# Kernel optimization log

Measured on AMD Instinct MI355X. Metric: run time of the kernel, lower is better.

Reference implementation:

```python
import jax, jax.numpy as jnp
import numpy as np

MIN_DISTANCE = 1.0  # default forward arg of the torch module


def setup_inputs() -> dict:
    key = jax.random.key(0)
    k1, k2 = jax.random.split(key)
    B, N = 4, 4096
    coords = jax.random.normal(k1, (B, N, 3), dtype=jnp.float32) * 5.0
    steric_radii = jax.random.uniform(k2, (B, N), dtype=jnp.float32)
    return {"coords": coords, "steric_radii": steric_radii}


def reference(coords, steric_radii):
    # coords: [B,N,3], steric_radii: [B,N]
    diff = coords[:, :, None, :] - coords[:, None, :, :]          # [B,N,N,3]
    d2 = jnp.sum(diff * diff, axis=-1)                             # [B,N,N]
    # safe sqrt: exact 0 on the diagonal (matches torch.cdist), no NaN grads
    pairwise = jnp.where(d2 > 0, jnp.sqrt(jnp.where(d2 > 0, d2, 1.0)), 0.0)
    sr = steric_radii[:, :, None] + steric_radii[:, None, :]       # [B,N,N]
    target = jnp.maximum(MIN_DISTANCE, sr)
    penalty = jax.nn.relu(target - pairwise)[..., None]            # [B,N,N,1]
    direction = jnp.clip(diff, -1.0, 1.0)                          # [B,N,N,3]
    adjustment = jnp.mean(penalty * direction, axis=2)             # [B,N,3]
    return coords + 0.1 * adjustment
```

## Files before the change

### kernel.cpp

```cpp
#include <hip/hip_runtime.h>

#define BB 4
#define NN 4096
#define TI 256
#define JB 32
#define JLEN (NN / JB)

#if __has_builtin(__builtin_amdgcn_sqrtf)
  #define FAST_SQRT __builtin_amdgcn_sqrtf
#else
  #define FAST_SQRT sqrtf
#endif

__device__ __forceinline__ float clip1(float x) {
    return fminf(fmaxf(x, -1.0f), 1.0f);
}

__global__ __launch_bounds__(TI) void ncp_partial(
    const float* __restrict__ coords,
    const float* __restrict__ radii,
    float* __restrict__ part)
{
    __shared__ float4 jt[JLEN];
    const int b = blockIdx.z;
    const int i = blockIdx.x * TI + threadIdx.x;
    const int s = blockIdx.y;
    const int jbase = s * JLEN;

    if (threadIdx.x < JLEN) {
        const int jj = jbase + threadIdx.x;
        jt[threadIdx.x] = make_float4(coords[(b * NN + jj) * 3 + 0],
                                      coords[(b * NN + jj) * 3 + 1],
                                      coords[(b * NN + jj) * 3 + 2],
                                      radii[b * NN + jj]);
    }

    const float xi = coords[(b * NN + i) * 3 + 0];
    const float yi = coords[(b * NN + i) * 3 + 1];
    const float zi = coords[(b * NN + i) * 3 + 2];
    const float ri = radii[b * NN + i];

    float ax = 0.0f, ay = 0.0f, az = 0.0f;

    __syncthreads();

    #pragma unroll 4
    for (int k = 0; k < JLEN; ++k) {
        const float4 c = jt[k];
        const float dx = xi - c.x;
        const float dy = yi - c.y;
        const float dz = zi - c.z;
        const float d2 = fmaf(dx, dx, fmaf(dy, dy, dz * dz));
        if (__any(d2 < 4.0f)) {
            const float dist = FAST_SQRT(d2);
            const float tgt = fmaxf(1.0f, ri + c.w);
            const float p = fmaxf(tgt - dist, 0.0f);
            ax = fmaf(p, clip1(dx), ax);
            ay = fmaf(p, clip1(dy), ay);
            az = fmaf(p, clip1(dz), az);
        }
    }

    float* dst = part + (size_t)s * (BB * NN * 3);
    const int o = (b * NN + i) * 3;
    dst[o + 0] = ax;
    dst[o + 1] = ay;
    dst[o + 2] = az;
}

__global__ __launch_bounds__(256) void ncp_reduce(
    const float* __restrict__ coords,
    const float* __restrict__ part,
    float* __restrict__ out)
{
    const int o = blockIdx.x * 256 + threadIdx.x;
    if (o >= BB * NN * 3) return;
    float acc = 0.0f;
    #pragma unroll
    for (int s = 0; s < JB; ++s)
        acc += part[(size_t)s * (BB * NN * 3) + o];
    out[o] = fmaf(0.1f / (float)NN, acc, coords[o]);
}

__global__ __launch_bounds__(TI) void ncp_direct(
    const float* __restrict__ coords,
    const float* __restrict__ radii,
    float* __restrict__ out)
{
    __shared__ float4 jt[TI];
    const int b = blockIdx.z;
    const int i = blockIdx.x * TI + threadIdx.x;

    const float xi = coords[(b * NN + i) * 3 + 0];
    const float yi = coords[(b * NN + i) * 3 + 1];
    const float zi = coords[(b * NN + i) * 3 + 2];
    const float ri = radii[b * NN + i];

    float ax = 0.0f, ay = 0.0f, az = 0.0f;

    for (int jc = 0; jc < NN; jc += TI) {
        const int jj = jc + threadIdx.x;
        __syncthreads();
        jt[threadIdx.x] = make_float4(coords[(b * NN + jj) * 3 + 0],
                                      coords[(b * NN + jj) * 3 + 1],
                                      coords[(b * NN + jj) * 3 + 2],
                                      radii[b * NN + jj]);
        __syncthreads();
        #pragma unroll 4
        for (int k = 0; k < TI; ++k) {
            const float4 c = jt[k];
            const float dx = xi - c.x;
            const float dy = yi - c.y;
            const float dz = zi - c.z;
            const float d2 = fmaf(dx, dx, fmaf(dy, dy, dz * dz));
            if (__any(d2 < 4.0f)) {
                const float dist = FAST_SQRT(d2);
                const float tgt = fmaxf(1.0f, ri + c.w);
                const float p = fmaxf(tgt - dist, 0.0f);
                ax = fmaf(p, clip1(dx), ax);
                ay = fmaf(p, clip1(dy), ay);
                az = fmaf(p, clip1(dz), az);
            }
        }
    }

    const int o = (b * NN + i) * 3;
    const float sc = 0.1f / (float)NN;
    out[o + 0] = fmaf(sc, ax, coords[o + 0]);
    out[o + 1] = fmaf(sc, ay, coords[o + 1]);
    out[o + 2] = fmaf(sc, az, coords[o + 2]);
}

extern "C" void kernel_launch(void* const* d_in, const int* in_sizes, int n_in,
                              void* d_out, int out_size, void* d_ws, size_t ws_size,
                              hipStream_t stream) {
    const float* coords = (const float*)d_in[0];
    const float* radii  = (const float*)d_in[1];
    float* out = (float*)d_out;
    const int n = BB * NN * 3;
    const size_t need = (size_t)JB * n * sizeof(float);

    if (ws_size >= need) {
        ncp_partial<<<dim3(NN / TI, JB, BB), TI, 0, stream>>>(
            coords, radii, (float*)d_ws);
        ncp_reduce<<<(n + 255) / 256, 256, 0, stream>>>(
            coords, (float*)d_ws, out);
    } else {
        ncp_direct<<<dim3(NN / TI, 1, BB), TI, 0, stream>>>(coords, radii, out);
    }
}
```

Before: 81.14 us.

## Pre-pack coords and radii into float4 buffer and read j-tiles directly from global

Adds a pack kernel that interleaves coords and radii into a float4 workspace array. The partial kernel then reads j-points straight from global memory through uniform float4 loads instead of staging them in LDS behind a __syncthreads. This removes the strided three-float gathers and the block barrier, at the cost of an extra kernel launch and more workspace use. Inner-loop loads now hit the cache instead of LDS.

```diff
diff --git a/kernel.cpp b/kernel.cpp
--- a/kernel.cpp
+++ b/kernel.cpp
@@ -16,37 +16,37 @@
     return fminf(fmaxf(x, -1.0f), 1.0f);
 }
 
-__global__ __launch_bounds__(TI) void ncp_partial(
+#define PACK_ELEMS (BB * NN)
+#define PART_OFF   (PACK_ELEMS * 4)
+
+__global__ __launch_bounds__(256) void ncp_pack(
     const float* __restrict__ coords,
     const float* __restrict__ radii,
+    float4* __restrict__ packed)
+{
+    const int t = blockIdx.x * 256 + threadIdx.x;
+    if (t >= PACK_ELEMS) return;
+    packed[t] = make_float4(coords[t * 3 + 0], coords[t * 3 + 1],
+                            coords[t * 3 + 2], radii[t]);
+}
+
+__global__ __launch_bounds__(TI) void ncp_partial(
+    const float4* __restrict__ packed,
     float* __restrict__ part)
 {
-    __shared__ float4 jt[JLEN];
     const int b = blockIdx.z;
     const int i = blockIdx.x * TI + threadIdx.x;
     const int s = blockIdx.y;
-    const int jbase = s * JLEN;
+    const float4* jsrc = packed + b * NN + s * JLEN;
 
-    if (threadIdx.x < JLEN) {
-        const int jj = jbase + threadIdx.x;
-        jt[threadIdx.x] = make_float4(coords[(b * NN + jj) * 3 + 0],
-                                      coords[(b * NN + jj) * 3 + 1],
-                                      coords[(b * NN + jj) * 3 + 2],
-                                      radii[b * NN + jj]);
-    }
-
-    const float xi = coords[(b * NN + i) * 3 + 0];
-    const float yi = coords[(b * NN + i) * 3 + 1];
-    const float zi = coords[(b * NN + i) * 3 + 2];
-    const float ri = radii[b * NN + i];
+    const float4 me = packed[b * NN + i];
+    const float xi = me.x, yi = me.y, zi = me.z, ri = me.w;
 
     float ax = 0.0f, ay = 0.0f, az = 0.0f;
 
-    __syncthreads();
-
     #pragma unroll 4
     for (int k = 0; k < JLEN; ++k) {
-        const float4 c = jt[k];
+        const float4 c = jsrc[k];
         const float dx = xi - c.x;
         const float dy = yi - c.y;
         const float dz = zi - c.z;
@@ -138,13 +138,14 @@
     const float* radii  = (const float*)d_in[1];
     float* out = (float*)d_out;
     const int n = BB * NN * 3;
-    const size_t need = (size_t)JB * n * sizeof(float);
+    const size_t need = (size_t)(PART_OFF + (size_t)JB * n) * sizeof(float);
 
     if (ws_size >= need) {
-        ncp_partial<<<dim3(NN / TI, JB, BB), TI, 0, stream>>>(
-            coords, radii, (float*)d_ws);
-        ncp_reduce<<<(n + 255) / 256, 256, 0, stream>>>(
-            coords, (float*)d_ws, out);
+        float4* packed = (float4*)d_ws;
+        float* part = (float*)d_ws + PART_OFF;
+        ncp_pack<<<(PACK_ELEMS + 255) / 256, 256, 0, stream>>>(coords, radii, packed);
+        ncp_partial<<<dim3(NN / TI, JB, BB), TI, 0, stream>>>(packed, part);
+        ncp_reduce<<<(n + 255) / 256, 256, 0, stream>>>(coords, part, out);
     } else {
         ncp_direct<<<dim3(NN / TI, 1, BB), TI, 0, stream>>>(coords, radii, out);
     }
```

Measured after the change: 81.12 us. About the same (-0.0%).

## Fuse partial and reduce kernels into one block-level j-split with shared-memory reduction

Applied to the files above, without the earlier changes.

Replaces the two-kernel scheme (per-slice partial sums to workspace, then a reduce kernel) with a single kernel. Each 1024-thread block stages all 4096 points of a batch in LDS, handles 32 i-points, and splits j across 32 half-wave streams. The partial sums are then combined in shared memory. This removes the second launch and the global workspace traffic, and makes each wavefront's __any branch cover only 32 i-points against contiguous j. The cost is that every block reloads the full 64KB point set, only 96 threads do the final reduction, and a 64KB LDS footprint plus large blocks may limit occupancy.

```diff
diff --git a/kernel.cpp b/kernel.cpp
--- a/kernel.cpp
+++ b/kernel.cpp
@@ -2,9 +2,10 @@
 
 #define BB 4
 #define NN 4096
-#define TI 256
-#define JB 32
-#define JLEN (NN / JB)
+#define TPB 1024
+#define STREAMS 32
+#define JPS (NN / STREAMS)
+#define GRP 4
 
 #if __has_builtin(__builtin_amdgcn_sqrtf)
   #define FAST_SQRT __builtin_amdgcn_sqrtf
@@ -16,107 +17,53 @@
     return fminf(fmaxf(x, -1.0f), 1.0f);
 }
 
-__global__ __launch_bounds__(TI) void ncp_partial(
-    const float* __restrict__ coords,
-    const float* __restrict__ radii,
-    float* __restrict__ part)
-{
-    __shared__ float4 jt[JLEN];
-    const int b = blockIdx.z;
-    const int i = blockIdx.x * TI + threadIdx.x;
-    const int s = blockIdx.y;
-    const int jbase = s * JLEN;
-
-    if (threadIdx.x < JLEN) {
-        const int jj = jbase + threadIdx.x;
-        jt[threadIdx.x] = make_float4(coords[(b * NN + jj) * 3 + 0],
-                                      coords[(b * NN + jj) * 3 + 1],
-                                      coords[(b * NN + jj) * 3 + 2],
-                                      radii[b * NN + jj]);
-    }
-
-    const float xi = coords[(b * NN + i) * 3 + 0];
-    const float yi = coords[(b * NN + i) * 3 + 1];
-    const float zi = coords[(b * NN + i) * 3 + 2];
-    const float ri = radii[b * NN + i];
-
-    float ax = 0.0f, ay = 0.0f, az = 0.0f;
-
-    __syncthreads();
-
-    #pragma unroll 4
-    for (int k = 0; k < JLEN; ++k) {
-        const float4 c = jt[k];
-        const float dx = xi - c.x;
-        const float dy = yi - c.y;
-        const float dz = zi - c.z;
-        const float d2 = fmaf(dx, dx, fmaf(dy, dy, dz * dz));
-        if (__any(d2 < 4.0f)) {
-            const float dist = FAST_SQRT(d2);
-            const float tgt = fmaxf(1.0f, ri + c.w);
-            const float p = fmaxf(tgt - dist, 0.0f);
-            ax = fmaf(p, clip1(dx), ax);
-            ay = fmaf(p, clip1(dy), ay);
-            az = fmaf(p, clip1(dz), az);
-        }
-    }
-
-    float* dst = part + (size_t)s * (BB * NN * 3);
-    const int o = (b * NN + i) * 3;
-    dst[o + 0] = ax;
-    dst[o + 1] = ay;
-    dst[o + 2] = az;
-}
-
-__global__ __launch_bounds__(256) void ncp_reduce(
-    const float* __restrict__ coords,
-    const float* __restrict__ part,
-    float* __restrict__ out)
-{
-    const int o = blockIdx.x * 256 + threadIdx.x;
-    if (o >= BB * NN * 3) return;
-    float acc = 0.0f;
-    #pragma unroll
-    for (int s = 0; s < JB; ++s)
-        acc += part[(size_t)s * (BB * NN * 3) + o];
-    out[o] = fmaf(0.1f / (float)NN, acc, coords[o]);
-}
-
-__global__ __launch_bounds__(TI) void ncp_direct(
+__global__ __launch_bounds__(TPB, 8) void ncp_one(
     const float* __restrict__ coords,
     const float* __restrict__ radii,
     float* __restrict__ out)
 {
-    __shared__ float4 jt[TI];
+    __shared__ __align__(16) char smem[65536];
+    float4* pts = (float4*)smem;
+    float*  red = (float*)smem;
+
     const int b = blockIdx.z;
-    const int i = blockIdx.x * TI + threadIdx.x;
+    const int ibase = blockIdx.x * 32;
 
-    const float xi = coords[(b * NN + i) * 3 + 0];
-    const float yi = coords[(b * NN + i) * 3 + 1];
-    const float zi = coords[(b * NN + i) * 3 + 2];
-    const float ri = radii[b * NN + i];
+    for (int p = threadIdx.x; p < NN; p += TPB) {
+        const int g = b * NN + p;
+        pts[p] = make_float4(coords[3 * g + 0], coords[3 * g + 1],
+                             coords[3 * g + 2], radii[g]);
+    }
+    __syncthreads();
+
+    const int l = threadIdx.x & 63;
+    const int li = l & 31;
+    const int half = l >> 5;
+    const int w = threadIdx.x >> 6;
+    const int stream = w * 2 + half;
+    const int i = ibase + li;
+
+    const float4 me = pts[i];
+    const float xi = me.x, yi = me.y, zi = me.z, ri = me.w;
+    const int jbase = stream * JPS;
 
     float ax = 0.0f, ay = 0.0f, az = 0.0f;
 
-    for (int jc = 0; jc < NN; jc += TI) {
-        const int jj = jc + threadIdx.x;
-        __syncthreads();
-        jt[threadIdx.x] = make_float4(coords[(b * NN + jj) * 3 + 0],
-                                      coords[(b * NN + jj) * 3 + 1],
-                                      coords[(b * NN + jj) * 3 + 2],
-                                      radii[b * NN + jj]);
-        __syncthreads();
-        #pragma unroll 4
-        for (int k = 0; k < TI; ++k) {
-            const float4 c = jt[k];
-            const float dx = xi - c.x;
-            const float dy = yi - c.y;
-            const float dz = zi - c.z;
+    for (int k0 = 0; k0 < JPS; k0 += GRP) {
+        float4 c[GRP];
+        #pragma unroll
+        for (int g = 0; g < GRP; ++g)
+            c[g] = pts[jbase + k0 + g];
+        #pragma unroll
+        for (int g = 0; g < GRP; ++g) {
+            const float dx = xi - c[g].x;
+            const float dy = yi - c[g].y;
+            const float dz = zi - c[g].z;
             const float d2 = fmaf(dx, dx, fmaf(dy, dy, dz * dz));
             if (__any(d2 < 4.0f)) {
                 const float dist = FAST_SQRT(d2);
-                const float tgt = fmaxf(1.0f, ri + c.w);
-                const float p = fmaxf(tgt - dist, 0.0f);
+                const float tgt  = fmaxf(1.0f, ri + c[g].w);
+                const float p    = fmaxf(tgt - dist, 0.0f);
                 ax = fmaf(p, clip1(dx), ax);
                 ay = fmaf(p, clip1(dy), ay);
                 az = fmaf(p, clip1(dz), az);
@@ -124,11 +71,23 @@
         }
     }
 
-    const int o = (b * NN + i) * 3;
-    const float sc = 0.1f / (float)NN;
-    out[o + 0] = fmaf(sc, ax, coords[o + 0]);
-    out[o + 1] = fmaf(sc, ay, coords[o + 1]);
-    out[o + 2] = fmaf(sc, az, coords[o + 2]);
+    __syncthreads();
+    const int rb = (stream * 32 + li) * 3;
+    red[rb + 0] = ax;
+    red[rb + 1] = ay;
+    red[rb + 2] = az;
+    __syncthreads();
+
+    if (threadIdx.x < 96) {
+        const int ii = threadIdx.x / 3;
+        const int comp = threadIdx.x % 3;
+        float acc = 0.0f;
+        #pragma unroll
+        for (int s = 0; s < STREAMS; ++s)
+            acc += red[(s * 32 + ii) * 3 + comp];
+        const int o = (b * NN + ibase + ii) * 3 + comp;
+        out[o] = fmaf(0.1f / (float)NN, acc, coords[o]);
+    }
 }
 
 extern "C" void kernel_launch(void* const* d_in, const int* in_sizes, int n_in,
@@ -137,15 +96,7 @@
     const float* coords = (const float*)d_in[0];
     const float* radii  = (const float*)d_in[1];
     float* out = (float*)d_out;
-    const int n = BB * NN * 3;
-    const size_t need = (size_t)JB * n * sizeof(float);
+    (void)d_ws; (void)ws_size;
 
-    if (ws_size >= need) {
-        ncp_partial<<<dim3(NN / TI, JB, BB), TI, 0, stream>>>(
-            coords, radii, (float*)d_ws);
-        ncp_reduce<<<(n + 255) / 256, 256, 0, stream>>>(
-            coords, (float*)d_ws, out);
-    } else {
-        ncp_direct<<<dim3(NN / TI, 1, BB), TI, 0, stream>>>(coords, radii, out);
-    }
+    ncp_one<<<dim3(NN / 32, 1, BB), TPB, 0, stream>>>(coords, radii, out);
 }
```

New measurement: 73.71 us. 9.2% less time.
